# Optimization experiments

Measured on AMD Instinct MI355X. Metric: run time of the kernel, lower is better.

## Reference

```python
import jax, jax.numpy as jnp
import numpy as np

B, H, S, HD = 4, 16, 4096, 64
DIM = 2 * HD
NF = 9
LAMBDA_INIT = 0.01


def setup_inputs() -> dict:
    key = jax.random.key(0)
    ks = jax.random.split(key, 8)
    shape = (B, H, S, HD)
    Q_t = jax.random.normal(ks[0], shape, jnp.float32)
    Q_prime_t = jax.random.normal(ks[1], shape, jnp.float32)
    K_t = jax.random.normal(ks[2], shape, jnp.float32)
    K_prime_t = jax.random.normal(ks[3], shape, jnp.float32)
    V = jax.random.normal(ks[4], shape, jnp.float32)
    lambdas = jnp.full((NF,), LAMBDA_INIT, jnp.float32)
    # xavier_uniform for [NF, DIM] linear weights
    bound = float(np.sqrt(6.0 / (NF + DIM)))
    Wq = jax.random.uniform(ks[5], (NF, DIM), jnp.float32, -bound, bound)
    Wk = jax.random.uniform(ks[6], (NF, DIM), jnp.float32, -bound, bound)
    return {"Q_t": Q_t, "Q_prime_t": Q_prime_t, "K_t": K_t,
            "K_prime_t": K_prime_t, "V": V,
            "lambdas": lambdas, "Wq": Wq, "Wk": Wk}


def _ste_argmax_route(scores):
    # forward: hard one-hot; backward: softmax gradient (straight-through)
    idx = jnp.argmax(scores, axis=-1)
    one_hot = jax.nn.one_hot(idx, scores.shape[-1], dtype=scores.dtype)
    soft = jax.nn.softmax(scores, axis=-1)
    return one_hot + soft - jax.lax.stop_gradient(soft)


def _lambda_for(x, x_prime, W, lambdas):
    cat = jax.lax.stop_gradient(jnp.concatenate([x, x_prime], axis=-1))  # [B,H,S,2hd]
    scores = jnp.einsum('bshd,nd->bshn'.replace('s', 'x'), cat, W)  # placeholder
    return scores


def reference(Q_t, Q_prime_t, K_t, K_prime_t, V, lambdas, Wq, Wk):
    # routing scores (routers see detached inputs)
    Q_cat = jax.lax.stop_gradient(jnp.concatenate([Q_t, Q_prime_t], axis=-1))  # [B,H,S,2hd]
    K_cat = jax.lax.stop_gradient(jnp.concatenate([K_t, K_prime_t], axis=-1))
    q_scores = jnp.einsum('bhsd,nd->bhsn', Q_cat, Wq)
    k_scores = jnp.einsum('bhsd,nd->bhsn', K_cat, Wk)
    q_route = _ste_argmax_route(q_scores)  # [B,H,S,NF]
    k_route = _ste_argmax_route(k_scores)
    lambda_q = jnp.sum(q_route * lambdas, axis=-1, keepdims=True)  # [B,H,S,1]
    lambda_k = jnp.sum(k_route * lambdas, axis=-1, keepdims=True)
    Q_diff = Q_t - lambda_q * Q_prime_t
    K_diff = K_t - lambda_k * K_prime_t
    KV = jnp.einsum('bhsd,bhse->bhde', K_diff, V)   # [B,H,hd,hd]
    O = jnp.einsum('bhsd,bhde->bhse', Q_diff, KV)   # [B,H,S,hd]
    return O
```

## Files before the change

kernel.cpp:

```cpp
#include <hip/hip_runtime.h>

#define Sx 4096
#define HDx 64
#define NF 9
#define NHEAD 64
#define NCH 16
#define SC (Sx / NCH)
#define NTILE (SC / 64)
#define LROW 72

typedef __attribute__((ext_vector_type(8))) short bf16x8;
typedef __attribute__((ext_vector_type(4))) float f32x4;

__device__ __forceinline__ unsigned short f2bf(float f) {
    union { float f; unsigned u; } x; x.f = f;
    unsigned r = x.u + 0x7fffu + ((x.u >> 16) & 1u);
    return (unsigned short)(r >> 16);
}
__device__ __forceinline__ float bf2f(unsigned short b) {
    union { unsigned u; float f; } x; x.u = ((unsigned)b) << 16;
    return x.f;
}
__device__ __forceinline__ unsigned long long pack4(float4 v) {
    return (unsigned long long)f2bf(v.x)
         | ((unsigned long long)f2bf(v.y) << 16)
         | ((unsigned long long)f2bf(v.z) << 32)
         | ((unsigned long long)f2bf(v.w) << 48);
}

__global__ __launch_bounds__(256) void kv_kernel(
    const float* __restrict__ Kt, const float* __restrict__ Kp,
    const float* __restrict__ V,  const float* __restrict__ lambdas,
    const float* __restrict__ Wk, float* __restrict__ KVt)
{
    __shared__ __align__(16) unsigned short kt_s[64][LROW];
    __shared__ __align__(16) unsigned short kp_s[64][LROW];
    __shared__ __align__(16) unsigned short kd_s[64][LROW];
    __shared__ float lam_s[64];
    __shared__ float lam9[16];

    const int tid  = threadIdx.x;
    const int lane = tid & 63;
    const int wave = tid >> 6;
    const int l15  = lane & 15;
    const int q    = lane >> 4;
    const int head  = blockIdx.x & (NHEAD - 1);
    const int chunk = blockIdx.x >> 6;
    const size_t hbase = (size_t)head * Sx * HDx;
    const int sbase = chunk * SC;

    if (tid < NF) lam9[tid] = lambdas[tid];

    bf16x8 wb[4];
#pragma unroll
    for (int h = 0; h < 4; ++h)
#pragma unroll
        for (int j = 0; j < 8; ++j) {
            float w = (l15 < NF) ? Wk[l15 * 128 + h * 32 + q * 8 + j] : 0.f;
            wb[h][j] = (short)f2bf(w);
        }

    f32x4 acc[4];
#pragma unroll
    for (int mt = 0; mt < 4; ++mt) acc[mt] = (f32x4){0.f, 0.f, 0.f, 0.f};

    const int tok = tid >> 2;
    const int fb  = (tid & 3) * 16;

    for (int t = 0; t < NTILE; ++t) {
        const int s0 = sbase + t * 64;
        const float4* pkt = (const float4*)(Kt + hbase + (size_t)(s0 + tok) * HDx + fb);
        const float4* pkp = (const float4*)(Kp + hbase + (size_t)(s0 + tok) * HDx + fb);
        float4 ka[4], kb[4];
#pragma unroll
        for (int i = 0; i < 4; ++i) { ka[i] = pkt[i]; kb[i] = pkp[i]; }
        const int ecol = wave * 16 + l15;
        float vv[16];
#pragma unroll
        for (int h = 0; h < 2; ++h)
#pragma unroll
            for (int j = 0; j < 8; ++j)
                vv[h * 8 + j] = V[hbase + (size_t)(s0 + h * 32 + q * 8 + j) * HDx + ecol];
#pragma unroll
        for (int i = 0; i < 4; ++i) {
            *(unsigned long long*)&kt_s[tok][fb + 4 * i] = pack4(ka[i]);
            *(unsigned long long*)&kp_s[tok][fb + 4 * i] = pack4(kb[i]);
        }
        __syncthreads();
        const int mrow = wave * 16 + l15;
        bf16x8 af[4];
        af[0] = *(const bf16x8*)&kt_s[mrow][q * 8];
        af[1] = *(const bf16x8*)&kt_s[mrow][32 + q * 8];
        af[2] = *(const bf16x8*)&kp_s[mrow][q * 8];
        af[3] = *(const bf16x8*)&kp_s[mrow][32 + q * 8];
        f32x4 sc = (f32x4){0.f, 0.f, 0.f, 0.f};
#pragma unroll
        for (int h = 0; h < 4; ++h)
            sc = __builtin_amdgcn_mfma_f32_16x16x32_bf16(af[h], wb[h], sc, 0, 0, 0);
        float lamr[4];
#pragma unroll
        for (int r = 0; r < 4; ++r) {
            float v = (l15 < NF) ? sc[r] : -3.4e38f;
            int idx = l15;
#pragma unroll
            for (int m = 1; m < 16; m <<= 1) {
                float ov = __shfl_xor(v, m, 16);
                int   oi = __shfl_xor(idx, m, 16);
                bool take = (ov > v) || (ov == v && oi < idx);
                v = take ? ov : v; idx = take ? oi : idx;
            }
            lamr[r] = lam9[idx];
        }
        if (l15 == 0) {
#pragma unroll
            for (int r = 0; r < 4; ++r) lam_s[wave * 16 + q * 4 + r] = lamr[r];
        }
        __syncthreads();
        {
            const float lam = lam_s[tok];
#pragma unroll
            for (int i = 0; i < 4; ++i) {
                const float* a = (const float*)&ka[i];
                const float* b = (const float*)&kb[i];
#pragma unroll
                for (int jj = 0; jj < 4; ++jj)
                    kd_s[fb + 4 * i + jj][tok] = f2bf(a[jj] - lam * b[jj]);
            }
        }
        __syncthreads();
#pragma unroll
        for (int h = 0; h < 2; ++h) {
            bf16x8 bv;
#pragma unroll
            for (int j = 0; j < 8; ++j) bv[j] = (short)f2bf(vv[h * 8 + j]);
#pragma unroll
            for (int mt = 0; mt < 4; ++mt) {
                bf16x8 ad = *(const bf16x8*)&kd_s[mt * 16 + l15][h * 32 + q * 8];
                acc[mt] = __builtin_amdgcn_mfma_f32_16x16x32_bf16(ad, bv, acc[mt], 0, 0, 0);
            }
        }
        __syncthreads();
    }
    float* kvh = KVt + head * (HDx * HDx);
#pragma unroll
    for (int mt = 0; mt < 4; ++mt)
#pragma unroll
        for (int r = 0; r < 4; ++r) {
            const int d = mt * 16 + q * 4 + r;
            const int e = wave * 16 + l15;
            atomicAdd(&kvh[e * 64 + d], acc[mt][r]);
        }
}

__global__ __launch_bounds__(256) void out_kernel(
    const float* __restrict__ Qt, const float* __restrict__ Qp,
    const float* __restrict__ lambdas, const float* __restrict__ Wq,
    const float* __restrict__ KVt, float* __restrict__ O)
{
    __shared__ __align__(16) unsigned short qt_s[64][LROW];
    __shared__ __align__(16) unsigned short qp_s[64][LROW];
    __shared__ float lam_s[64];
    __shared__ float lam9[16];

    const int tid  = threadIdx.x;
    const int lane = tid & 63;
    const int wave = tid >> 6;
    const int l15  = lane & 15;
    const int q    = lane >> 4;
    const int head  = blockIdx.x & (NHEAD - 1);
    const int chunk = blockIdx.x >> 6;
    const size_t hbase = (size_t)head * Sx * HDx;
    const int sbase = chunk * SC;

    if (tid < NF) lam9[tid] = lambdas[tid];

    bf16x8 wb[4];
#pragma unroll
    for (int h = 0; h < 4; ++h)
#pragma unroll
        for (int j = 0; j < 8; ++j) {
            float w = (l15 < NF) ? Wq[l15 * 128 + h * 32 + q * 8 + j] : 0.f;
            wb[h][j] = (short)f2bf(w);
        }

    bf16x8 bkv[4][2];
    const float* kvh = KVt + head * (HDx * HDx);
#pragma unroll
    for (int nt = 0; nt < 4; ++nt)
#pragma unroll
        for (int h = 0; h < 2; ++h)
#pragma unroll
            for (int j = 0; j < 8; ++j)
                bkv[nt][h][j] = (short)f2bf(kvh[(nt * 16 + l15) * 64 + h * 32 + q * 8 + j]);

    const int tok = tid >> 2;
    const int fb  = (tid & 3) * 16;

    for (int t = 0; t < NTILE; ++t) {
        const int s0 = sbase + t * 64;
        const float4* pqt = (const float4*)(Qt + hbase + (size_t)(s0 + tok) * HDx + fb);
        const float4* pqp = (const float4*)(Qp + hbase + (size_t)(s0 + tok) * HDx + fb);
        float4 qa[4], qb[4];
#pragma unroll
        for (int i = 0; i < 4; ++i) { qa[i] = pqt[i]; qb[i] = pqp[i]; }
#pragma unroll
        for (int i = 0; i < 4; ++i) {
            *(unsigned long long*)&qt_s[tok][fb + 4 * i] = pack4(qa[i]);
            *(unsigned long long*)&qp_s[tok][fb + 4 * i] = pack4(qb[i]);
        }
        __syncthreads();
        const int mrow = wave * 16 + l15;
        bf16x8 af[4];
        af[0] = *(const bf16x8*)&qt_s[mrow][q * 8];
        af[1] = *(const bf16x8*)&qt_s[mrow][32 + q * 8];
        af[2] = *(const bf16x8*)&qp_s[mrow][q * 8];
        af[3] = *(const bf16x8*)&qp_s[mrow][32 + q * 8];
        f32x4 sc = (f32x4){0.f, 0.f, 0.f, 0.f};
#pragma unroll
        for (int h = 0; h < 4; ++h)
            sc = __builtin_amdgcn_mfma_f32_16x16x32_bf16(af[h], wb[h], sc, 0, 0, 0);
        float lamr[4];
#pragma unroll
        for (int r = 0; r < 4; ++r) {
            float v = (l15 < NF) ? sc[r] : -3.4e38f;
            int idx = l15;
#pragma unroll
            for (int m = 1; m < 16; m <<= 1) {
                float ov = __shfl_xor(v, m, 16);
                int   oi = __shfl_xor(idx, m, 16);
                bool take = (ov > v) || (ov == v && oi < idx);
                v = take ? ov : v; idx = take ? oi : idx;
            }
            lamr[r] = lam9[idx];
        }
        if (l15 == 0) {
#pragma unroll
            for (int r = 0; r < 4; ++r) lam_s[wave * 16 + q * 4 + r] = lamr[r];
        }
        __syncthreads();
        const float lamv = lam_s[mrow];
        f32x4 oacc[4];
#pragma unroll
        for (int nt = 0; nt < 4; ++nt) oacc[nt] = (f32x4){0.f, 0.f, 0.f, 0.f};
#pragma unroll
        for (int h = 0; h < 2; ++h) {
            bf16x8 ad;
#pragma unroll
            for (int j = 0; j < 8; ++j) {
                float qd = bf2f((unsigned short)af[h][j])
                         - lamv * bf2f((unsigned short)af[2 + h][j]);
                ad[j] = (short)f2bf(qd);
            }
#pragma unroll
            for (int nt = 0; nt < 4; ++nt)
                oacc[nt] = __builtin_amdgcn_mfma_f32_16x16x32_bf16(ad, bkv[nt][h], oacc[nt], 0, 0, 0);
        }
#pragma unroll
        for (int nt = 0; nt < 4; ++nt)
#pragma unroll
            for (int r = 0; r < 4; ++r) {
                const int row = s0 + wave * 16 + q * 4 + r;
                O[hbase + (size_t)row * HDx + nt * 16 + l15] = oacc[nt][r];
            }
        __syncthreads();
    }
}

extern "C" void kernel_launch(void* const* d_in, const int* in_sizes, int n_in,
                              void* d_out, int out_size, void* d_ws, size_t ws_size,
                              hipStream_t stream) {
    const float* Qt      = (const float*)d_in[0];
    const float* Qp      = (const float*)d_in[1];
    const float* Kt      = (const float*)d_in[2];
    const float* Kp      = (const float*)d_in[3];
    const float* V       = (const float*)d_in[4];
    const float* lambdas = (const float*)d_in[5];
    const float* Wq      = (const float*)d_in[6];
    const float* Wk      = (const float*)d_in[7];
    float* O  = (float*)d_out;
    float* KV = (float*)d_ws;

    hipMemsetAsync(d_ws, 0, (size_t)NHEAD * HDx * HDx * sizeof(float), stream);
    kv_kernel <<<NHEAD * NCH, 256, 0, stream>>>(Kt, Kp, V, lambdas, Wk, KV);
    out_kernel<<<NHEAD * NCH, 256, 0, stream>>>(Qt, Qp, lambdas, Wq, KV, O);
}
```

Measured before the change: 367.9 us.

## Load K/Q straight into MFMA fragments, prefetch next tile, regrid both kernels

Drops the shared-memory staging of K/K' and Q/Q'. Each lane now loads its MFMA A-fragment directly from global memory and broadcasts lambda with shuffles instead of through shared memory, which removes two barriers per tile. The KV kernel prefetches the next tile's K, K' and V into registers while the current tile is computed, and uses twice as many chunks. The output kernel processes one 64-token tile per block across 4096 blocks. The goal is lower sync and LDS overhead and better latency hiding, at the cost of higher register pressure and twice as many atomics on KV.

New measurement: 417.7 us. 13.5% more time.

```diff
diff --git a/kernel.cpp b/kernel.cpp
--- a/kernel.cpp
+++ b/kernel.cpp
@@ -1,12 +1,14 @@
 #include <hip/hip_runtime.h>
+
 
 #define Sx 4096
 #define HDx 64
 #define NF 9
 #define NHEAD 64
-#define NCH 16
-#define SC (Sx / NCH)
-#define NTILE (SC / 64)
+#define NCHK 32
+#define SCK (Sx / NCHK)
+#define NTK (SCK / 64)
+#define NCHO 64
 #define LROW 72
 
 typedef __attribute__((ext_vector_type(8))) short bf16x8;
@@ -21,22 +23,44 @@
     union { unsigned u; float f; } x; x.u = ((unsigned)b) << 16;
     return x.f;
 }
-__device__ __forceinline__ unsigned long long pack4(float4 v) {
-    return (unsigned long long)f2bf(v.x)
-         | ((unsigned long long)f2bf(v.y) << 16)
-         | ((unsigned long long)f2bf(v.z) << 32)
-         | ((unsigned long long)f2bf(v.w) << 48);
-}
-
-__global__ __launch_bounds__(256) void kv_kernel(
+__device__ __forceinline__ bf16x8 pack8(float4 a, float4 b) {
+    bf16x8 r;
+    r[0] = (short)f2bf(a.x); r[1] = (short)f2bf(a.y);
+    r[2] = (short)f2bf(a.z); r[3] = (short)f2bf(a.w);
+    r[4] = (short)f2bf(b.x); r[5] = (short)f2bf(b.y);
+    r[6] = (short)f2bf(b.z); r[7] = (short)f2bf(b.w);
+    return r;
+}
+
+__device__ __forceinline__ float route_lam(float v, int l15, const float* lam9) {
+    int idx = l15;
+#pragma unroll
+    for (int m = 1; m < 16; m <<= 1) {
+        float ov = __shfl_xor(v, m, 16);
+        int   oi = __shfl_xor(idx, m, 16);
+        bool take = (ov > v) || (ov == v && oi < idx);
+        v = take ? ov : v; idx = take ? oi : idx;
+    }
+    return lam9[idx];
+}
+
+__device__ __forceinline__ float lam_bcast(float r0, float r1, float r2, float r3, int l15) {
+    const int src = ((l15 >> 2) << 4) + l15;
+    float t0 = __shfl(r0, src);
+    float t1 = __shfl(r1, src);
+    float t2 = __shfl(r2, src);
+    float t3 = __shfl(r3, src);
+    float lo = (l15 & 1) ? t1 : t0;
+    float hi = (l15 & 1) ? t3 : t2;
+    return (l15 & 2) ? hi : lo;
+}
+
+__global__ __launch_bounds__(256, 4) void kv_kernel(
     const float* __restrict__ Kt, const float* __restrict__ Kp,
     const float* __restrict__ V,  const float* __restrict__ lambdas,
     const float* __restrict__ Wk, float* __restrict__ KVt)
 {
-    __shared__ __align__(16) unsigned short kt_s[64][LROW];
-    __shared__ __align__(16) unsigned short kp_s[64][LROW];
     __shared__ __align__(16) unsigned short kd_s[64][LROW];
-    __shared__ float lam_s[64];
     __shared__ float lam9[16];
 
     const int tid  = threadIdx.x;
@@ -47,7 +71,8 @@
     const int head  = blockIdx.x & (NHEAD - 1);
     const int chunk = blockIdx.x >> 6;
     const size_t hbase = (size_t)head * Sx * HDx;
-    const int sbase = chunk * SC;
+    const int sbase = chunk * SCK;
+    const int myrow = wave * 16 + l15;
 
     if (tid < NF) lam9[tid] = lambdas[tid];
 
@@ -64,83 +89,86 @@
 #pragma unroll
     for (int mt = 0; mt < 4; ++mt) acc[mt] = (f32x4){0.f, 0.f, 0.f, 0.f};
 
-    const int tok = tid >> 2;
-    const int fb  = (tid & 3) * 16;
-
-    for (int t = 0; t < NTILE; ++t) {
-        const int s0 = sbase + t * 64;
-        const float4* pkt = (const float4*)(Kt + hbase + (size_t)(s0 + tok) * HDx + fb);
-        const float4* pkp = (const float4*)(Kp + hbase + (size_t)(s0 + tok) * HDx + fb);
-        float4 ka[4], kb[4];
-#pragma unroll
-        for (int i = 0; i < 4; ++i) { ka[i] = pkt[i]; kb[i] = pkp[i]; }
-        const int ecol = wave * 16 + l15;
-        float vv[16];
-#pragma unroll
-        for (int h = 0; h < 2; ++h)
-#pragma unroll
-            for (int j = 0; j < 8; ++j)
-                vv[h * 8 + j] = V[hbase + (size_t)(s0 + h * 32 + q * 8 + j) * HDx + ecol];
-#pragma unroll
-        for (int i = 0; i < 4; ++i) {
-            *(unsigned long long*)&kt_s[tok][fb + 4 * i] = pack4(ka[i]);
-            *(unsigned long long*)&kp_s[tok][fb + 4 * i] = pack4(kb[i]);
-        }
-        __syncthreads();
-        const int mrow = wave * 16 + l15;
-        bf16x8 af[4];
-        af[0] = *(const bf16x8*)&kt_s[mrow][q * 8];
-        af[1] = *(const bf16x8*)&kt_s[mrow][32 + q * 8];
-        af[2] = *(const bf16x8*)&kp_s[mrow][q * 8];
-        af[3] = *(const bf16x8*)&kp_s[mrow][32 + q * 8];
+    const float* kt0 = Kt + hbase + (size_t)(sbase + myrow) * HDx + q * 8;
+    const float* kp0 = Kp + hbase + (size_t)(sbase + myrow) * HDx + q * 8;
+    float4 a0 = *(const float4*)(kt0),      a1 = *(const float4*)(kt0 + 4);
+    float4 a2 = *(const float4*)(kt0 + 32), a3 = *(const float4*)(kt0 + 36);
+    float4 b0 = *(const float4*)(kp0),      b1 = *(const float4*)(kp0 + 4);
+    float4 b2 = *(const float4*)(kp0 + 32), b3 = *(const float4*)(kp0 + 36);
+    float vv[16];
+#pragma unroll
+    for (int h = 0; h < 2; ++h)
+#pragma unroll
+        for (int j = 0; j < 8; ++j)
+            vv[h * 8 + j] = V[hbase + (size_t)(sbase + h * 32 + q * 8 + j) * HDx + wave * 16 + l15];
+
+    __syncthreads();
+
+    bf16x8 af[4];
+    af[0] = pack8(a0, a1); af[1] = pack8(a2, a3);
+    af[2] = pack8(b0, b1); af[3] = pack8(b2, b3);
+
+#pragma unroll
+    for (int t = 0; t < NTK; ++t) {
         f32x4 sc = (f32x4){0.f, 0.f, 0.f, 0.f};
 #pragma unroll
         for (int h = 0; h < 4; ++h)
             sc = __builtin_amdgcn_mfma_f32_16x16x32_bf16(af[h], wb[h], sc, 0, 0, 0);
-        float lamr[4];
-#pragma unroll
-        for (int r = 0; r < 4; ++r) {
-            float v = (l15 < NF) ? sc[r] : -3.4e38f;
-            int idx = l15;
-#pragma unroll
-            for (int m = 1; m < 16; m <<= 1) {
-                float ov = __shfl_xor(v, m, 16);
-                int   oi = __shfl_xor(idx, m, 16);
-                bool take = (ov > v) || (ov == v && oi < idx);
-                v = take ? ov : v; idx = take ? oi : idx;
-            }
-            lamr[r] = lam9[idx];
-        }
-        if (l15 == 0) {
-#pragma unroll
-            for (int r = 0; r < 4; ++r) lam_s[wave * 16 + q * 4 + r] = lamr[r];
-        }
+        float lr0 = route_lam((l15 < NF) ? sc[0] : -3.4e38f, l15, lam9);
+        float lr1 = route_lam((l15 < NF) ? sc[1] : -3.4e38f, l15, lam9);
+        float lr2 = route_lam((l15 < NF) ? sc[2] : -3.4e38f, l15, lam9);
+        float lr3 = route_lam((l15 < NF) ? sc[3] : -3.4e38f, l15, lam9);
+        const float lam = lam_bcast(lr0, lr1, lr2, lr3, l15);
+
+#pragma unroll
+        for (int h = 0; h < 2; ++h)
+#pragma unroll
+            for (int j = 0; j < 8; ++j)
+                kd_s[h * 32 + q * 8 + j][myrow] =
+                    f2bf(bf2f((unsigned short)af[h][j]) - lam * bf2f((unsigned short)af[2 + h][j]));
+
+        float4 na0, na1, na2, na3, nb0, nb1, nb2, nb3;
+        float nvv[16];
+        if (t + 1 < NTK) {
+            const int s0n = sbase + (t + 1) * 64;
+            const float* ktn = Kt + hbase + (size_t)(s0n + myrow) * HDx + q * 8;
+            const float* kpn = Kp + hbase + (size_t)(s0n + myrow) * HDx + q * 8;
+            na0 = *(const float4*)(ktn);      na1 = *(const float4*)(ktn + 4);
+            na2 = *(const float4*)(ktn + 32); na3 = *(const float4*)(ktn + 36);
+            nb0 = *(const float4*)(kpn);      nb1 = *(const float4*)(kpn + 4);
+            nb2 = *(const float4*)(kpn + 32); nb3 = *(const float4*)(kpn + 36);
+#pragma unroll
+            for (int h = 0; h < 2; ++h)
+#pragma unroll
+                for (int j = 0; j < 8; ++j)
+                    nvv[h * 8 + j] = V[hbase + (size_t)(s0n + h * 32 + q * 8 + j) * HDx + wave * 16 + l15];
+        }
+
+        bf16x8 bv[2];
+#pragma unroll
+        for (int h = 0; h < 2; ++h)
+#pragma unroll
+            for (int j = 0; j < 8; ++j) bv[h][j] = (short)f2bf(vv[h * 8 + j]);
+
         __syncthreads();
-        {
-            const float lam = lam_s[tok];
-#pragma unroll
-            for (int i = 0; i < 4; ++i) {
-                const float* a = (const float*)&ka[i];
-                const float* b = (const float*)&kb[i];
-#pragma unroll
-                for (int jj = 0; jj < 4; ++jj)
-                    kd_s[fb + 4 * i + jj][tok] = f2bf(a[jj] - lam * b[jj]);
-            }
-        }
-        __syncthreads();
-#pragma unroll
-        for (int h = 0; h < 2; ++h) {
-            bf16x8 bv;
-#pragma unroll
-            for (int j = 0; j < 8; ++j) bv[j] = (short)f2bf(vv[h * 8 + j]);
+
+#pragma unroll
+        for (int h = 0; h < 2; ++h)
 #pragma unroll
             for (int mt = 0; mt < 4; ++mt) {
                 bf16x8 ad = *(const bf16x8*)&kd_s[mt * 16 + l15][h * 32 + q * 8];
-                acc[mt] = __builtin_amdgcn_mfma_f32_16x16x32_bf16(ad, bv, acc[mt], 0, 0, 0);
+                acc[mt] = __builtin_amdgcn_mfma_f32_16x16x32_bf16(ad, bv[h], acc[mt], 0, 0, 0);
             }
-        }
-        __syncthreads();
+
+        if (t + 1 < NTK) {
+            __syncthreads();
+            af[0] = pack8(na0, na1); af[1] = pack8(na2, na3);
+            af[2] = pack8(nb0, nb1); af[3] = pack8(nb2, nb3);
+#pragma unroll
+            for (int j = 0; j < 16; ++j) vv[j] = nvv[j];
+        }
     }
+
     float* kvh = KVt + head * (HDx * HDx);
 #pragma unroll
     for (int mt = 0; mt < 4; ++mt)
@@ -152,14 +180,11 @@
         }
 }
 
-__global__ __launch_bounds__(256) void out_kernel(
+__global__ __launch_bounds__(256, 4) void out_kernel(
     const float* __restrict__ Qt, const float* __restrict__ Qp,
     const float* __restrict__ lambdas, const float* __restrict__ Wq,
     const float* __restrict__ KVt, float* __restrict__ O)
 {
-    __shared__ __align__(16) unsigned short qt_s[64][LROW];
-    __shared__ __align__(16) unsigned short qp_s[64][LROW];
-    __shared__ float lam_s[64];
     __shared__ float lam9[16];
 
     const int tid  = threadIdx.x;
@@ -170,9 +195,17 @@
     const int head  = blockIdx.x & (NHEAD - 1);
     const int chunk = blockIdx.x >> 6;
     const size_t hbase = (size_t)head * Sx * HDx;
-    const int sbase = chunk * SC;
+    const int s0 = chunk * 64;
+    const int myrow = wave * 16 + l15;
 
     if (tid < NF) lam9[tid] = lambdas[tid];
+
+    const float* qt0 = Qt + hbase + (size_t)(s0 + myrow) * HDx + q * 8;
+    const float* qp0 = Qp + hbase + (size_t)(s0 + myrow) * HDx + q * 8;
+    float4 a0 = *(const float4*)(qt0),      a1 = *(const float4*)(qt0 + 4);
+    float4 a2 = *(const float4*)(qt0 + 32), a3 = *(const float4*)(qt0 + 36);
+    float4 b0 = *(const float4*)(qp0),      b1 = *(const float4*)(qp0 + 4);
+    float4 b2 = *(const float4*)(qp0 + 32), b3 = *(const float4*)(qp0 + 36);
 
     bf16x8 wb[4];
 #pragma unroll
@@ -188,82 +221,51 @@
 #pragma unroll
     for (int nt = 0; nt < 4; ++nt)
 #pragma unroll
-        for (int h = 0; h < 2; ++h)
-#pragma unroll
-            for (int j = 0; j < 8; ++j)
-                bkv[nt][h][j] = (short)f2bf(kvh[(nt * 16 + l15) * 64 + h * 32 + q * 8 + j]);
-
-    const int tok = tid >> 2;
-    const int fb  = (tid & 3) * 16;
-
-    for (int t = 0; t < NTILE; ++t) {
-        const int s0 = sbase + t * 64;
-        const float4* pqt = (const float4*)(Qt + hbase + (size_t)(s0 + tok) * HDx + fb);
-        const float4* pqp = (const float4*)(Qp + hbase + (size_t)(s0 + tok) * HDx + fb);
-        float4 qa[4], qb[4];
-#pragma unroll
-        for (int i = 0; i < 4; ++i) { qa[i] = pqt[i]; qb[i] = pqp[i]; }
-#pragma unroll
-        for (int i = 0; i < 4; ++i) {
-            *(unsigned long long*)&qt_s[tok][fb + 4 * i] = pack4(qa[i]);
-            *(unsigned long long*)&qp_s[tok][fb + 4 * i] = pack4(qb[i]);
-        }
-        __syncthreads();
-        const int mrow = wave * 16 + l15;
-        bf16x8 af[4];
-        af[0] = *(const bf16x8*)&qt_s[mrow][q * 8];
-        af[1] = *(const bf16x8*)&qt_s[mrow][32 + q * 8];
-        af[2] = *(const bf16x8*)&qp_s[mrow][q * 8];
-        af[3] = *(const bf16x8*)&qp_s[mrow][32 + q * 8];
-        f32x4 sc = (f32x4){0.f, 0.f, 0.f, 0.f};
-#pragma unroll
-        for (int h = 0; h < 4; ++h)
-            sc = __builtin_amdgcn_mfma_f32_16x16x32_bf16(af[h], wb[h], sc, 0, 0, 0);
-        float lamr[4];
+        for (int h = 0; h < 2; ++h) {
+            const float* p = &kvh[(nt * 16 + l15) * 64 + h * 32 + q * 8];
+            bkv[nt][h] = pack8(*(const float4*)p, *(const float4*)(p + 4));
+        }
+
+    __syncthreads();
+
+    bf16x8 af[4];
+    af[0] = pack8(a0, a1); af[1] = pack8(a2, a3);
+    af[2] = pack8(b0, b1); af[3] = pack8(b2, b3);
+
+    f32x4 sc = (f32x4){0.f, 0.f, 0.f, 0.f};
+#pragma unroll
+    for (int h = 0; h < 4; ++h)
+        sc = __builtin_amdgcn_mfma_f32_16x16x32_bf16(af[h], wb[h], sc, 0, 0, 0);
+    float lr0 = route_lam((l15 < NF) ? sc[0] : -3.4e38f, l15, lam9);
+    float lr1 = route_lam((l15 < NF) ? sc[1] : -3.4e38f, l15, lam9);
+    float lr2 = route_lam((l15 < NF) ? sc[2] : -3.4e38f, l15, lam9);
+    float lr3 = route_lam((l15 < NF) ? sc[3] : -3.4e38f, l15, lam9);
+    const float lam = lam_bcast(lr0, lr1, lr2, lr3, l15);
+
+    bf16x8 ad[2];
+#pragma unroll
+    for (int h = 0; h < 2; ++h)
+#pragma unroll
+        for (int j = 0; j < 8; ++j)
+            ad[h][j] = (short)f2bf(bf2f((unsigned short)af[h][j])
+                                   - lam * bf2f((unsigned short)af[2 + h][j]));
+
+    f32x4 oacc[4];
+#pragma unroll
+    for (int nt = 0; nt < 4; ++nt) oacc[nt] = (f32x4){0.f, 0.f, 0.f, 0.f};
+#pragma unroll
+    for (int h = 0; h < 2; ++h)
+#pragma unroll
+        for (int nt = 0; nt < 4; ++nt)
+            oacc[nt] = __builtin_amdgcn_mfma_f32_16x16x32_bf16(ad[h], bkv[nt][h], oacc[nt], 0, 0, 0);
+
+#pragma unroll
+    for (int nt = 0; nt < 4; ++nt)
 #pragma unroll
         for (int r = 0; r < 4; ++r) {
-            float v = (l15 < NF) ? sc[r] : -3.4e38f;
-            int idx = l15;
-#pragma unroll
-            for (int m = 1; m < 16; m <<= 1) {
-                float ov = __shfl_xor(v, m, 16);
-                int   oi = __shfl_xor(idx, m, 16);
-                bool take = (ov > v) || (ov == v && oi < idx);
-                v = take ? ov : v; idx = take ? oi : idx;
-            }
-            lamr[r] = lam9[idx];
-        }
-        if (l15 == 0) {
-#pragma unroll
-            for (int r = 0; r < 4; ++r) lam_s[wave * 16 + q * 4 + r] = lamr[r];
-        }
-        __syncthreads();
-        const float lamv = lam_s[mrow];
-        f32x4 oacc[4];
-#pragma unroll
-        for (int nt = 0; nt < 4; ++nt) oacc[nt] = (f32x4){0.f, 0.f, 0.f, 0.f};
-#pragma unroll
-        for (int h = 0; h < 2; ++h) {
-            bf16x8 ad;
-#pragma unroll
-            for (int j = 0; j < 8; ++j) {
-                float qd = bf2f((unsigned short)af[h][j])
-                         - lamv * bf2f((unsigned short)af[2 + h][j]);
-                ad[j] = (short)f2bf(qd);
-            }
-#pragma unroll
-            for (int nt = 0; nt < 4; ++nt)
-                oacc[nt] = __builtin_amdgcn_mfma_f32_16x16x32_bf16(ad, bkv[nt][h], oacc[nt], 0, 0, 0);
-        }
-#pragma unroll
-        for (int nt = 0; nt < 4; ++nt)
-#pragma unroll
-            for (int r = 0; r < 4; ++r) {
-                const int row = s0 + wave * 16 + q * 4 + r;
-                O[hbase + (size_t)row * HDx + nt * 16 + l15] = oacc[nt][r];
-            }
-        __syncthreads();
-    }
+            const int row = s0 + wave * 16 + q * 4 + r;
+            O[hbase + (size_t)row * HDx + nt * 16 + l15] = oacc[nt][r];
+        }
 }
 
 extern "C" void kernel_launch(void* const* d_in, const int* in_sizes, int n_in,
@@ -281,6 +283,6 @@
     float* KV = (float*)d_ws;
 
     hipMemsetAsync(d_ws, 0, (size_t)NHEAD * HDx * HDx * sizeof(float), stream);
-    kv_kernel <<<NHEAD * NCH, 256, 0, stream>>>(Kt, Kp, V, lambdas, Wk, KV);
-    out_kernel<<<NHEAD * NCH, 256, 0, stream>>>(Qt, Qp, lambdas, Wq, KV, O);
-}
+    kv_kernel <<<NHEAD * NCHK, 256, 0, stream>>>(Kt, Kp, V, lambdas, Wk, KV);
+    out_kernel<<<NHEAD * NCHO, 256, 0, stream>>>(Qt, Qp, lambdas, Wq, KV, O);
+}
```
